# Performance work log

Measured on AMD Instinct MI355X. Metric: run time of the kernel, lower is better.

## Reference

```python
import jax, jax.numpy as jnp
import numpy as np

D_MODEL = 96
N_HEAD = 3
HEAD_DIM = D_MODEL // N_HEAD  # 32
D_FF = 2048
WIDTH = 65
HALF_W = (WIDTH - 1) // 2  # 32
EPS = 1e-5


def layer_norm(x, g, b):
    mu = jnp.mean(x, axis=-1, keepdims=True)
    var = jnp.mean(jnp.square(x - mu), axis=-1, keepdims=True)
    return (x - mu) * jax.lax.rsqrt(var + EPS) * g + b


def setup_inputs() -> dict:
    key = jax.random.key(0)
    ks = jax.random.split(key, 8)
    B, T = 8, 2048
    s = 0.05
    return {
        "x": jax.random.normal(ks[0], (B, D_MODEL, T), dtype=jnp.float32),
        "w_qkv": jax.random.normal(ks[1], (3 * D_MODEL, D_MODEL), dtype=jnp.float32) * s,
        "b_qkv": jnp.zeros((3 * D_MODEL,), dtype=jnp.float32),
        "w_out": jax.random.normal(ks[2], (D_MODEL, D_MODEL), dtype=jnp.float32) * s,
        "b_out": jnp.zeros((D_MODEL,), dtype=jnp.float32),
        "ln1_g": jnp.ones((D_MODEL,), dtype=jnp.float32),
        "ln1_b": jnp.zeros((D_MODEL,), dtype=jnp.float32),
        "w_ff1": jax.random.normal(ks[3], (D_FF, D_MODEL), dtype=jnp.float32) * s,
        "b_ff1": jnp.zeros((D_FF,), dtype=jnp.float32),
        "w_ff2": jax.random.normal(ks[4], (D_MODEL, D_FF), dtype=jnp.float32) * s,
        "b_ff2": jnp.zeros((D_MODEL,), dtype=jnp.float32),
        "ln2_g": jnp.ones((D_MODEL,), dtype=jnp.float32),
        "ln2_b": jnp.zeros((D_MODEL,), dtype=jnp.float32),
        "lnf_g": jnp.ones((D_MODEL,), dtype=jnp.float32),
        "lnf_b": jnp.zeros((D_MODEL,), dtype=jnp.float32),
    }


def reference(x, w_qkv, b_qkv, w_out, b_out, ln1_g, ln1_b, w_ff1, b_ff1,
              w_ff2, b_ff2, ln2_g, ln2_b, lnf_g, lnf_b):
    # x: (B, C, T) -> (B, T, C)
    h = jnp.transpose(x, (0, 2, 1))
    B, T, C = h.shape

    # --- multi-head self-attention with banded mask ---
    qkv = h @ w_qkv.T + b_qkv                      # (B, T, 3C)
    q, k, v = jnp.split(qkv, 3, axis=-1)
    q = q.reshape(B, T, N_HEAD, HEAD_DIM)
    k = k.reshape(B, T, N_HEAD, HEAD_DIM)
    v = v.reshape(B, T, N_HEAD, HEAD_DIM)

    scale = 1.0 / jnp.sqrt(jnp.float32(HEAD_DIM))
    scores = jnp.einsum("bthd,bshd->bhts", q, k) * scale  # (B, H, T, T)

    idx = jnp.arange(T)
    band = jnp.abs(idx[:, None] - idx[None, :]) <= HALF_W  # |i-j| <= half width
    scores = jnp.where(band[None, None], scores, jnp.float32(-jnp.inf))

    attn = jax.nn.softmax(scores, axis=-1)
    ctx = jnp.einsum("bhts,bshd->bthd", attn, v).reshape(B, T, C)
    attn_out = ctx @ w_out.T + b_out

    # --- post-norm encoder layer (dropout inactive / eval mode) ---
    h = layer_norm(h + attn_out, ln1_g, ln1_b)
    ff = jax.nn.relu(h @ w_ff1.T + b_ff1) @ w_ff2.T + b_ff2
    h = layer_norm(h + ff, ln2_g, ln2_b)

    # extra layernorm applied when width is not None
    h = layer_norm(h, lnf_g, lnf_b)

    # (B, T, C) -> (B, C, T)
    return jnp.transpose(h, (0, 2, 1))
```

## Files before the change

### kernel.cpp

```cpp
#include <hip/hip_runtime.h>
#include <hip/hip_bf16.h>

#define B 8
#define T 2048
#define C 96
#define NH 3
#define HD 32
#define FFD 2048
#define HALF_W 32
#define BT (B*T)
#define NT 384

typedef __hip_bfloat16 bf16;
typedef __attribute__((ext_vector_type(8))) short short8;
typedef __attribute__((ext_vector_type(4))) short short4v;
typedef __attribute__((ext_vector_type(16))) float floatx16;

__device__ __forceinline__ short f2bs(float v){
    __hip_bfloat16 h = __float2bfloat16(v);
    return *reinterpret_cast<short*>(&h);
}
__device__ __forceinline__ float bs2f(short s){
    unsigned u = ((unsigned)(unsigned short)s) << 16;
    return __uint_as_float(u);
}
__device__ __forceinline__ short8 ld_b64x2(const short* p){
    short4v a = *(const short4v*)p;
    short4v b = *(const short4v*)(p + 4);
    short8 v;
    v[0]=a[0]; v[1]=a[1]; v[2]=a[2]; v[3]=a[3];
    v[4]=b[0]; v[5]=b[1]; v[6]=b[2]; v[7]=b[3];
    return v;
}
__device__ __forceinline__ int4 exch_pair(int a0,int a1,int b0,int b1,int hq){
    int ra0=__shfl_xor(a0,32), ra1=__shfl_xor(a1,32);
    int rb0=__shfl_xor(b0,32), rb1=__shfl_xor(b1,32);
    int4 s;
    s.x = hq ? rb0 : a0;
    s.y = hq ? rb1 : a1;
    s.z = hq ? b0  : ra0;
    s.w = hq ? b1  : ra1;
    return s;
}
__device__ __forceinline__ void proj_pack(const floatx16& acc, const float* bias32, int hq,
                                          short8& f0, short8& f1){
    int pkq[4][2];
    #pragma unroll
    for(int q = 0; q < 4; ++q){
        float4 bv = *(const float4*)(bias32 + 8*q + 4*hq);
        short4v t;
        t[0]=f2bs(acc[4*q+0]+bv.x); t[1]=f2bs(acc[4*q+1]+bv.y);
        t[2]=f2bs(acc[4*q+2]+bv.z); t[3]=f2bs(acc[4*q+3]+bv.w);
        int2 u = *(int2*)&t; pkq[q][0]=u.x; pkq[q][1]=u.y;
    }
    int4 r0 = exch_pair(pkq[0][0],pkq[0][1],pkq[1][0],pkq[1][1],hq);
    int4 r1 = exch_pair(pkq[2][0],pkq[2][1],pkq[3][0],pkq[3][1],hq);
    f0 = *(short8*)&r0; f1 = *(short8*)&r1;
}

__global__ void cvtw_kernel(const float* __restrict__ wq, const float* __restrict__ wo,
                            const float* __restrict__ w1, const float* __restrict__ w2,
                            bf16* __restrict__ dst){
    int i = blockIdx.x*256 + threadIdx.x;
    if(i < 27648){
        int e = i&7, lane = (i>>3)&63, r = i>>9;
        int ks = r%6, ot = r/6;
        int o = ot*32 + (lane&31);
        int k = ks*16 + (lane>>5)*8 + e;
        dst[i] = __float2bfloat16(wq[o*96 + k]);
    } else if(i < 36864){
        int j = i - 27648;
        int e = j&7, lane = (j>>3)&63, r = j>>9;
        int ks = r%6, ct = r/6;
        int c = ct*32 + (lane&31);
        int k = ks*16 + (lane>>5)*8 + e;
        dst[i] = __float2bfloat16(wo[c*96 + k]);
    } else if(i < 233472){
        int j = i - 36864;
        int e = j&7, lane = (j>>3)&63, r = j>>9;
        int ks = r%6; r /= 6;
        int w = r%4, jt = r/4;
        int row = jt*128 + w*32 + (lane&31);
        int k = ks*16 + (lane>>5)*8 + e;
        dst[i] = __float2bfloat16(w1[row*96 + k]);
    } else if(i < 430080){
        int j = i - 233472;
        int e = j&7, lane = (j>>3)&63, r = j>>9;
        int ct = r%3; r /= 3;
        int g = r%2; r /= 2;
        int w = r%4, jt = r/4;
        int c = ct*32 + (lane&31);
        int k = jt*128 + w*32 + g*16 + (lane>>5)*8 + e;
        dst[i] = __float2bfloat16(w2[c*FFD + k]);
    }
}

__global__ __launch_bounds__(384, 3) void encoder_kernel(
    const float* __restrict__ x,
    const bf16* __restrict__ wqs, const bf16* __restrict__ wos,
    const bf16* __restrict__ w1s, const bf16* __restrict__ w2s,
    const float* __restrict__ b_qkv, const float* __restrict__ b_out,
    const float* __restrict__ g1, const float* __restrict__ bb1,
    const float* __restrict__ b1, const float* __restrict__ b2,
    const float* __restrict__ g2, const float* __restrict__ bt2,
    const float* __restrict__ gf, const float* __restrict__ btf,
    float* __restrict__ out){
    __shared__ __align__(16) char smem[59392];
    short* XS   = (short*)smem;
    short* PTS  = (short*)smem;
    float* REDP = (float*)smem;
    short* VTS  = (short*)(smem + 26112);
    float* ZT   = (float*)(smem + 26112);
    short* CTX  = (short*)(smem + 45312);
    short* H1S  = (short*)(smem + 51712);
    float* LSS  = (float*)(smem + 58112);
    float* RED1 = (float*)(smem + 58496);

    const int tid = threadIdx.x;
    const int u = tid >> 6, lane = tid & 63;
    const int lm = lane & 31, hq = lane >> 5;
    const int grp = u / 3, h = u % 3;
    const int b  = blockIdx.x >> 6;
    const int tt = blockIdx.x & 63;
    const int t0 = tt * 32;
    const float* xb = x + (size_t)b*C*T;

    int tg0 = t0 - 32;
    if(tg0 >= 0 && t0 + 64 <= T){
        for(int e = tid; e < 96*24; e += NT){
            int c = e / 24, t4 = e % 24;
            float4 v = *(const float4*)(xb + (size_t)c*T + tg0 + t4*4);
            XS[(t4*4+0)*104 + c] = f2bs(v.x);
            XS[(t4*4+1)*104 + c] = f2bs(v.y);
            XS[(t4*4+2)*104 + c] = f2bs(v.z);
            XS[(t4*4+3)*104 + c] = f2bs(v.w);
        }
    } else {
        for(int e = tid; e < 96*96; e += NT){
            int c = e / 96, j = e % 96;
            int t = tg0 + j; t = t < 0 ? 0 : (t > T-1 ? T-1 : t);
            XS[j*104 + c] = f2bs(xb[(size_t)c*T + t]);
        }
    }
    __syncthreads();

    short8 kf[3][2], qf0, qf1, wof[6];
    if(grp == 0){
        short8 kwf[6];
        #pragma unroll
        for(int ks = 0; ks < 6; ++ks)
            kwf[ks] = *(const short8*)((const short*)wqs + (size_t)((3+h)*6 + ks)*512 + lane*8);
        #pragma unroll
        for(int tau = 0; tau < 3; ++tau){
            short8 bfr[6];
            #pragma unroll
            for(int ks = 0; ks < 6; ++ks)
                bfr[ks] = *(const short8*)(XS + (tau*32+lm)*104 + ks*16 + hq*8);
            floatx16 acc;
            #pragma unroll
            for(int r = 0; r < 16; ++r) acc[r] = 0.f;
            #pragma unroll
            for(int ks = 0; ks < 6; ++ks)
                acc = __builtin_amdgcn_mfma_f32_32x32x16_bf16(kwf[ks], bfr[ks], acc, 0,0,0);
            proj_pack(acc, b_qkv + (3+h)*32, hq, kf[tau][0], kf[tau][1]);
            if(tau == 1){
                floatx16 qa;
                #pragma unroll
                for(int r = 0; r < 16; ++r) qa[r] = 0.f;
                #pragma unroll
                for(int ks = 0; ks < 6; ++ks){
                    short8 qwf = *(const short8*)((const short*)wqs + (size_t)(h*6 + ks)*512 + lane*8);
                    qa = __builtin_amdgcn_mfma_f32_32x32x16_bf16(qwf, bfr[ks], qa, 0,0,0);
                }
                proj_pack(qa, b_qkv + h*32, hq, qf0, qf1);
            }
        }
        #pragma unroll
        for(int ks = 0; ks < 6; ++ks)
            wof[ks] = *(const short8*)((const short*)wos + (size_t)(h*6 + ks)*512 + lane*8);
    } else {
        short8 vwf[6];
        #pragma unroll
        for(int ks = 0; ks < 6; ++ks)
            vwf[ks] = *(const short8*)((const short*)wqs + (size_t)((6+h)*6 + ks)*512 + lane*8);
        #pragma unroll
        for(int tau = 0; tau < 3; ++tau){
            short8 bfr[6];
            #pragma unroll
            for(int ks = 0; ks < 6; ++ks)
                bfr[ks] = *(const short8*)(XS + (tau*32+lm)*104 + ks*16 + hq*8);
            floatx16 acc;
            #pragma unroll
            for(int r = 0; r < 16; ++r) acc[r] = 0.f;
            #pragma unroll
            for(int ks = 0; ks < 6; ++ks)
                acc = __builtin_amdgcn_mfma_f32_32x32x16_bf16(vwf[ks], bfr[ks], acc, 0,0,0);
            #pragma unroll
            for(int q = 0; q < 4; ++q){
                float4 bv = *(const float4*)(b_qkv + (6+h)*32 + 8*q + 4*hq);
                float bva[4] = {bv.x, bv.y, bv.z, bv.w};
                #pragma unroll
                for(int r = 0; r < 4; ++r)
                    VTS[h*3200 + (8*q + 4*hq + r)*100 + tau*32 + lm] = f2bs(acc[4*q+r] + bva[r]);
            }
        }
    }
    __syncthreads();

    if(grp == 0){
        floatx16 S[3];
        #pragma unroll
        for(int sub = 0; sub < 3; ++sub){
            floatx16 z;
            #pragma unroll
            for(int r = 0; r < 16; ++r) z[r] = 0.f;
            z = __builtin_amdgcn_mfma_f32_32x32x16_bf16(kf[sub][0], qf0, z, 0,0,0);
            z = __builtin_amdgcn_mfma_f32_32x32x16_bf16(kf[sub][1], qf1, z, 0,0,0);
            S[sub] = z;
        }
        const float scale = 0.17677669529663687f;
        float part = 0.f;
        #pragma unroll
        for(int sub = 0; sub < 3; ++sub){
            #pragma unroll
            for(int r = 0; r < 16; ++r){
                int key_local = sub*32 + (r&3) + 8*(r>>2) + 4*hq;
                int s_glob = t0 - 32 + key_local;
                int rel = key_local - lm;
                bool ok = (rel >= 0) && (rel <= 64) && (s_glob >= 0) && (s_glob < T);
                float p = ok ? __expf(S[sub][r]*scale) : 0.f;
                S[sub][r] = p;
                part += p;
            }
        }
        float ltot = part + __shfl_xor(part, 32);
        if(hq == 0) LSS[h*32 + lm] = ltot;
        #pragma unroll
        for(int sub = 0; sub < 3; ++sub){
            #pragma unroll
            for(int q4 = 0; q4 < 4; ++q4){
                int kbase = sub*32 + 8*q4 + 4*hq;
                short4v pk4;
                pk4[0] = f2bs(S[sub][4*q4+0]);
                pk4[1] = f2bs(S[sub][4*q4+1]);
                pk4[2] = f2bs(S[sub][4*q4+2]);
                pk4[3] = f2bs(S[sub][4*q4+3]);
                *(short4v*)(PTS + h*3200 + lm*100 + kbase) = pk4;
            }
        }
        floatx16 O;
        #pragma unroll
        for(int r = 0; r < 16; ++r) O[r] = 0.f;
        #pragma unroll
        for(int ks = 0; ks < 6; ++ks){
            short8 pa = ld_b64x2(PTS + h*3200 + lm*100 + ks*16 + hq*8);
            short8 vf = ld_b64x2(VTS + h*3200 + lm*100 + ks*16 + hq*8);
            O = __builtin_amdgcn_mfma_f32_32x32x16_bf16(pa, vf, O, 0,0,0);
        }
        #pragma unroll
        for(int r = 0; r < 16; ++r){
            int qr = (r&3) + 8*(r>>2) + 4*hq;
            float linv = 1.f / LSS[h*32 + qr];
            CTX[qr*100 + h*32 + lm] = f2bs(O[r]*linv);
        }
    }
    __syncthreads();

    float vals[16];
    if(grp == 0){
        short8 cbfr[6];
        #pragma unroll
        for(int ks = 0; ks < 6; ++ks)
            cbfr[ks] = ld_b64x2(CTX + lm*100 + ks*16 + hq*8);
        floatx16 pacc;
        #pragma unroll
        for(int r = 0; r < 16; ++r) pacc[r] = 0.f;
        #pragma unroll
        for(int ks = 0; ks < 6; ++ks)
            pacc = __builtin_amdgcn_mfma_f32_32x32x16_bf16(wof[ks], cbfr[ks], pacc, 0,0,0);
        float p1 = 0.f, p2 = 0.f;
        #pragma unroll
        for(int q = 0; q < 4; ++q){
            int c = h*32 + 8*q + 4*hq;
            float4 bv = *(const float4*)(b_out + c);
            float bva[4] = {bv.x, bv.y, bv.z, bv.w};
            #pragma unroll
            for(int r = 0; r < 4; ++r){
                float xv = xb[(size_t)(c + r)*T + t0 + lm];
                float v = pacc[4*q+r] + bva[r] + xv;
                vals[4*q+r] = v;
                p1 += v; p2 += v*v;
            }
        }
        p1 += __shfl_xor(p1, 32);
        p2 += __shfl_xor(p2, 32);
        if(hq == 0){ RED1[h*32 + lm] = p1; RED1[96 + h*32 + lm] = p2; }
    }
    __syncthreads();
    if(grp == 0){
        float s  = RED1[lm] + RED1[32 + lm] + RED1[64 + lm];
        float s2 = RED1[96 + lm] + RED1[128 + lm] + RED1[160 + lm];
        float mu = s * (1.0f/96.0f);
        float rstd = rsqrtf(s2*(1.0f/96.0f) - mu*mu + 1e-5f);
        #pragma unroll
        for(int q = 0; q < 4; ++q){
            int c = h*32 + 8*q + 4*hq;
            float4 gv = *(const float4*)(g1 + c);
            float4 bv = *(const float4*)(bb1 + c);
            float ga[4] = {gv.x, gv.y, gv.z, gv.w};
            float ba[4] = {bv.x, bv.y, bv.z, bv.w};
            short4v pkv;
            #pragma unroll
            for(int r = 0; r < 4; ++r)
                pkv[r] = f2bs((vals[4*q+r] - mu)*rstd*ga[r] + ba[r]);
            *(short4v*)(H1S + lm*100 + c) = pkv;
        }
    }
    __syncthreads();

    short8 hf[6];
    #pragma unroll
    for(int ks = 0; ks < 6; ++ks)
        hf[ks] = ld_b64x2(H1S + lm*100 + ks*16 + hq*8);
    floatx16 acc2[3];
    #pragma unroll
    for(int i = 0; i < 3; ++i)
        #pragma unroll
        for(int r = 0; r < 16; ++r) acc2[i][r] = 0.f;
    const short* w1b = (const short*)w1s + lane*8;
    const short* w2b = (const short*)w2s + lane*8;
    short8 cw1[6];
    #pragma unroll
    for(int ks = 0; ks < 6; ++ks)
        cw1[ks] = *(const short8*)(w1b + (size_t)(u*6 + ks)*512);
    const int nJ = (u < 4) ? 11 : 10;
    for(int it = 0; it < nJ; ++it){
        const int J  = u + it*6;
        const int Jn = (J + 6 < 64) ? J + 6 : u;
        short8 nw1[6];
        #pragma unroll
        for(int ks = 0; ks < 6; ++ks)
            nw1[ks] = *(const short8*)(w1b + (size_t)(Jn*6 + ks)*512);
        short8 w2f[6];
        #pragma unroll
        for(int g = 0; g < 2; ++g)
            #pragma unroll
            for(int ct = 0; ct < 3; ++ct)
                w2f[g*3 + ct] = *(const short8*)(w2b + (size_t)((J*2 + g)*3 + ct)*512);
        floatx16 a0;
        #pragma unroll
        for(int r = 0; r < 16; ++r) a0[r] = 0.f;
        #pragma unroll
        for(int ks = 0; ks < 6; ++ks)
            a0 = __builtin_amdgcn_mfma_f32_32x32x16_bf16(cw1[ks], hf[ks], a0, 0,0,0);
        int pk[4][2];
        #pragma unroll
        for(int q = 0; q < 4; ++q){
            float4 bv = *(const float4*)(b1 + J*32 + 8*q + 4*hq);
            float bva[4] = {bv.x, bv.y, bv.z, bv.w};
            short4v tv;
            #pragma unroll
            for(int r = 0; r < 4; ++r){
                float v0 = a0[4*q+r] + bva[r];
                tv[r] = f2bs(v0 > 0.f ? v0 : 0.f);
            }
            int2 uu = *(int2*)&tv; pk[q][0] = uu.x; pk[q][1] = uu.y;
        }
        #pragma unroll
        for(int g = 0; g < 2; ++g){
            int4 sfi = exch_pair(pk[2*g][0], pk[2*g][1], pk[2*g+1][0], pk[2*g+1][1], hq);
            short8 sf = *(short8*)&sfi;
            #pragma unroll
            for(int ct = 0; ct < 3; ++ct)
                acc2[ct] = __builtin_amdgcn_mfma_f32_32x32x16_bf16(w2f[g*3+ct], sf, acc2[ct], 0,0,0);
        }
        #pragma unroll
        for(int ks = 0; ks < 6; ++ks) cw1[ks] = nw1[ks];
    }

    float fv[16];
    float e1 = 0.f, e2 = 0.f;
    for(int s = 0; s < 3; ++s){
        #pragma unroll
        for(int q = 0; q < 4; ++q)
            #pragma unroll
            for(int r = 0; r < 4; ++r)
                REDP[u*1088 + lane*17 + 4*q + r] = acc2[s][4*q+r];
        __syncthreads();
        if(u == s){
            #pragma unroll
            for(int q = 0; q < 4; ++q){
                int c = s*32 + 8*q + 4*hq;
                float4 bv = *(const float4*)(b2 + c);
                float bva[4] = {bv.x, bv.y, bv.z, bv.w};
                #pragma unroll
                for(int r = 0; r < 4; ++r){
                    float v = REDP[0*1088 + lane*17 + 4*q + r]
                            + REDP[1*1088 + lane*17 + 4*q + r]
                            + REDP[2*1088 + lane*17 + 4*q + r]
                            + REDP[3*1088 + lane*17 + 4*q + r]
                            + REDP[4*1088 + lane*17 + 4*q + r]
                            + REDP[5*1088 + lane*17 + 4*q + r]
                            + bva[r] + bs2f(H1S[lm*100 + c + r]);
                    fv[4*q+r] = v;
                    e1 += v; e2 += v*v;
                }
            }
        }
        __syncthreads();
    }
    if(grp == 0){
        e1 += __shfl_xor(e1, 32);
        e2 += __shfl_xor(e2, 32);
        if(hq == 0){ RED1[h*32 + lm] = e1; RED1[96 + h*32 + lm] = e2; }
    }
    __syncthreads();
    float f1 = 0.f, f2 = 0.f;
    if(grp == 0){
        float s  = RED1[lm] + RED1[32 + lm] + RED1[64 + lm];
        float s2 = RED1[96 + lm] + RED1[128 + lm] + RED1[160 + lm];
        float mu = s * (1.0f/96.0f);
        float rstd = rsqrtf(s2*(1.0f/96.0f) - mu*mu + 1e-5f);
        #pragma unroll
        for(int q = 0; q < 4; ++q){
            int c = h*32 + 8*q + 4*hq;
            float4 gv = *(const float4*)(g2 + c);
            float4 bv = *(const float4*)(bt2 + c);
            float ga[4] = {gv.x, gv.y, gv.z, gv.w};
            float ba[4] = {bv.x, bv.y, bv.z, bv.w};
            #pragma unroll
            for(int r = 0; r < 4; ++r){
                float y = (fv[4*q+r] - mu)*rstd*ga[r] + ba[r];
                fv[4*q+r] = y;
                f1 += y; f2 += y*y;
            }
        }
        f1 += __shfl_xor(f1, 32);
        f2 += __shfl_xor(f2, 32);
    }
    __syncthreads();
    if(grp == 0 && hq == 0){ RED1[h*32 + lm] = f1; RED1[96 + h*32 + lm] = f2; }
    __syncthreads();
    if(grp == 0){
        float s  = RED1[lm] + RED1[32 + lm] + RED1[64 + lm];
        float s2 = RED1[96 + lm] + RED1[128 + lm] + RED1[160 + lm];
        float mu = s * (1.0f/96.0f);
        float rstd = rsqrtf(s2*(1.0f/96.0f) - mu*mu + 1e-5f);
        #pragma unroll
        for(int q = 0; q < 4; ++q){
            int c = h*32 + 8*q + 4*hq;
            float4 gv = *(const float4*)(gf + c);
            float4 bv = *(const float4*)(btf + c);
            float ga[4] = {gv.x, gv.y, gv.z, gv.w};
            float ba[4] = {bv.x, bv.y, bv.z, bv.w};
            #pragma unroll
            for(int r = 0; r < 4; ++r)
                ZT[(c + r)*36 + lm] = (fv[4*q+r] - mu)*rstd*ga[r] + ba[r];
        }
    }
    __syncthreads();
    float* ob = out + (size_t)b*C*T + t0;
    for(int e = tid; e < 96*8; e += NT){
        int c = e >> 3, qq = e & 7;
        *(float4*)(ob + (size_t)c*T + qq*4) = *(const float4*)(ZT + c*36 + qq*4);
    }
}

extern "C" void kernel_launch(void* const* d_in, const int* in_sizes, int n_in,
                              void* d_out, int out_size, void* d_ws, size_t ws_size,
                              hipStream_t stream) {
    const float* x     = (const float*)d_in[0];
    const float* w_qkv = (const float*)d_in[1];
    const float* b_qkv = (const float*)d_in[2];
    const float* w_out = (const float*)d_in[3];
    const float* b_out = (const float*)d_in[4];
    const float* ln1_g = (const float*)d_in[5];
    const float* ln1_b = (const float*)d_in[6];
    const float* w_ff1 = (const float*)d_in[7];
    const float* b_ff1 = (const float*)d_in[8];
    const float* w_ff2 = (const float*)d_in[9];
    const float* b_ff2 = (const float*)d_in[10];
    const float* ln2_g = (const float*)d_in[11];
    const float* ln2_b = (const float*)d_in[12];
    const float* lnf_g = (const float*)d_in[13];
    const float* lnf_b = (const float*)d_in[14];
    float* out = (float*)d_out;

    bf16* wts = (bf16*)d_ws;
    bf16* wqs = wts;
    bf16* wos = wts + 27648;
    bf16* w1s = wts + 36864;
    bf16* w2s = wts + 233472;

    cvtw_kernel   <<<1680, 256, 0, stream>>>(w_qkv, w_out, w_ff1, w_ff2, wts);
    encoder_kernel<<<B*(T/32), NT, 0, stream>>>(x, wqs, wos, w1s, w2s,
                                                b_qkv, b_out, ln1_g, ln1_b,
                                                b_ff1, b_ff2, ln2_g, ln2_b,
                                                lnf_g, lnf_b, out);
}
```

Measured before the change: 135.7 us.

## Double block to 12 waves, split QKV work and reduce FFN partials via atomics

Raises the block from 6 to 12 waves, with four waves per head that share the K, Q and V projections, staging K in shared memory. The FFN hidden tiles are spread across 12 waves, so each wave handles about half as many. The cross-wave reduction of FFN outputs now uses shared-memory atomicAdd into a zeroed buffer instead of three staged reduction rounds with barriers, and the shared-memory footprint shrinks. The aim is more parallelism per tile and fewer barriers. In exchange it adds LDS atomic contention, extra syncs, and pressure from launch_bounds(768,6) on registers.

```diff
diff --git a/kernel.cpp b/kernel.cpp
--- a/kernel.cpp
+++ b/kernel.cpp
@@ -9,7 +9,7 @@
 #define FFD 2048
 #define HALF_W 32
 #define BT (B*T)
-#define NT 384
+#define NT 768
 
 typedef __hip_bfloat16 bf16;
 typedef __attribute__((ext_vector_type(8))) short short8;
@@ -95,7 +95,7 @@
     }
 }
 
-__global__ __launch_bounds__(384, 3) void encoder_kernel(
+__global__ __launch_bounds__(768, 6) void encoder_kernel(
     const float* __restrict__ x,
     const bf16* __restrict__ wqs, const bf16* __restrict__ wos,
     const bf16* __restrict__ w1s, const bf16* __restrict__ w2s,
@@ -105,21 +105,22 @@
     const float* __restrict__ g2, const float* __restrict__ bt2,
     const float* __restrict__ gf, const float* __restrict__ btf,
     float* __restrict__ out){
-    __shared__ __align__(16) char smem[59392];
+    __shared__ __align__(16) char smem[53120];
     short* XS   = (short*)smem;
     short* PTS  = (short*)smem;
-    float* REDP = (float*)smem;
-    short* VTS  = (short*)(smem + 26112);
-    float* ZT   = (float*)(smem + 26112);
-    short* CTX  = (short*)(smem + 45312);
-    short* H1S  = (short*)(smem + 51712);
-    float* LSS  = (float*)(smem + 58112);
-    float* RED1 = (float*)(smem + 58496);
+    short* KS   = (short*)(smem + 19968);
+    short* CTX  = (short*)(smem + 19968);
+    short* H1S  = (short*)(smem + 26368);
+    short* VTS  = (short*)(smem + 32768);
+    float* FVS  = (float*)(smem + 32768);
+    float* ZT   = (float*)(smem + 32768);
+    float* LSS  = (float*)(smem + 51968);
+    float* RED1 = (float*)(smem + 52352);
 
     const int tid = threadIdx.x;
     const int u = tid >> 6, lane = tid & 63;
     const int lm = lane & 31, hq = lane >> 5;
-    const int grp = u / 3, h = u % 3;
+    const int p = u & 3, h = u >> 2;
     const int b  = blockIdx.x >> 6;
     const int tt = blockIdx.x & 63;
     const int t0 = tt * 32;
@@ -144,14 +145,21 @@
     }
     __syncthreads();
 
-    short8 kf[3][2], qf0, qf1, wof[6];
-    if(grp == 0){
+    short8 wof[6];
+    if(u < 3){
+        #pragma unroll
+        for(int ks = 0; ks < 6; ++ks)
+            wof[ks] = *(const short8*)((const short*)wos + (size_t)(u*6 + ks)*512 + lane*8);
+    }
+
+    short8 kf2[2], qf0, qf1;
+    if(p == 0){
         short8 kwf[6];
         #pragma unroll
         for(int ks = 0; ks < 6; ++ks)
             kwf[ks] = *(const short8*)((const short*)wqs + (size_t)((3+h)*6 + ks)*512 + lane*8);
         #pragma unroll
-        for(int tau = 0; tau < 3; ++tau){
+        for(int tau = 0; tau < 2; ++tau){
             short8 bfr[6];
             #pragma unroll
             for(int ks = 0; ks < 6; ++ks)
@@ -162,29 +170,54 @@
             #pragma unroll
             for(int ks = 0; ks < 6; ++ks)
                 acc = __builtin_amdgcn_mfma_f32_32x32x16_bf16(kwf[ks], bfr[ks], acc, 0,0,0);
-            proj_pack(acc, b_qkv + (3+h)*32, hq, kf[tau][0], kf[tau][1]);
-            if(tau == 1){
-                floatx16 qa;
-                #pragma unroll
-                for(int r = 0; r < 16; ++r) qa[r] = 0.f;
-                #pragma unroll
-                for(int ks = 0; ks < 6; ++ks){
-                    short8 qwf = *(const short8*)((const short*)wqs + (size_t)(h*6 + ks)*512 + lane*8);
-                    qa = __builtin_amdgcn_mfma_f32_32x32x16_bf16(qwf, bfr[ks], qa, 0,0,0);
-                }
-                proj_pack(qa, b_qkv + h*32, hq, qf0, qf1);
-            }
-        }
-        #pragma unroll
-        for(int ks = 0; ks < 6; ++ks)
-            wof[ks] = *(const short8*)((const short*)wos + (size_t)(h*6 + ks)*512 + lane*8);
+            short8 f0, f1;
+            proj_pack(acc, b_qkv + (3+h)*32, hq, f0, f1);
+            short* kp = KS + (size_t)(h*2 + tau)*1024 + lane*8;
+            *(short8*)kp = f0;
+            *(short8*)(kp + 512) = f1;
+        }
+    } else if(p == 1){
+        short8 kwf[6];
+        #pragma unroll
+        for(int ks = 0; ks < 6; ++ks)
+            kwf[ks] = *(const short8*)((const short*)wqs + (size_t)((3+h)*6 + ks)*512 + lane*8);
+        {
+            short8 bfr[6];
+            #pragma unroll
+            for(int ks = 0; ks < 6; ++ks)
+                bfr[ks] = *(const short8*)(XS + (2*32+lm)*104 + ks*16 + hq*8);
+            floatx16 acc;
+            #pragma unroll
+            for(int r = 0; r < 16; ++r) acc[r] = 0.f;
+            #pragma unroll
+            for(int ks = 0; ks < 6; ++ks)
+                acc = __builtin_amdgcn_mfma_f32_32x32x16_bf16(kwf[ks], bfr[ks], acc, 0,0,0);
+            proj_pack(acc, b_qkv + (3+h)*32, hq, kf2[0], kf2[1]);
+        }
+        {
+            short8 bfr[6];
+            #pragma unroll
+            for(int ks = 0; ks < 6; ++ks)
+                bfr[ks] = *(const short8*)(XS + (1*32+lm)*104 + ks*16 + hq*8);
+            floatx16 qa;
+            #pragma unroll
+            for(int r = 0; r < 16; ++r) qa[r] = 0.f;
+            #pragma unroll
+            for(int ks = 0; ks < 6; ++ks){
+                short8 qwf = *(const short8*)((const short*)wqs + (size_t)(h*6 + ks)*512 + lane*8);
+                qa = __builtin_amdgcn_mfma_f32_32x32x16_bf16(qwf, bfr[ks], qa, 0,0,0);
+            }
+            proj_pack(qa, b_qkv + h*32, hq, qf0, qf1);
+        }
     } else {
         short8 vwf[6];
         #pragma unroll
         for(int ks = 0; ks < 6; ++ks)
             vwf[ks] = *(const short8*)((const short*)wqs + (size_t)((6+h)*6 + ks)*512 + lane*8);
-        #pragma unroll
-        for(int tau = 0; tau < 3; ++tau){
+        const int taua = (p == 2) ? 0 : 2;
+        const int ntau = (p == 2) ? 2 : 1;
+        for(int i = 0; i < ntau; ++i){
+            int tau = taua + i;
             short8 bfr[6];
             #pragma unroll
             for(int ks = 0; ks < 6; ++ks)
@@ -207,15 +240,22 @@
     }
     __syncthreads();
 
-    if(grp == 0){
+    float on[16];
+    if(p == 1){
         floatx16 S[3];
         #pragma unroll
         for(int sub = 0; sub < 3; ++sub){
+            short8 ka, kb;
+            if(sub < 2){
+                const short* kp = KS + (size_t)(h*2 + sub)*1024 + lane*8;
+                ka = *(const short8*)kp;
+                kb = *(const short8*)(kp + 512);
+            } else { ka = kf2[0]; kb = kf2[1]; }
             floatx16 z;
             #pragma unroll
             for(int r = 0; r < 16; ++r) z[r] = 0.f;
-            z = __builtin_amdgcn_mfma_f32_32x32x16_bf16(kf[sub][0], qf0, z, 0,0,0);
-            z = __builtin_amdgcn_mfma_f32_32x32x16_bf16(kf[sub][1], qf1, z, 0,0,0);
+            z = __builtin_amdgcn_mfma_f32_32x32x16_bf16(ka, qf0, z, 0,0,0);
+            z = __builtin_amdgcn_mfma_f32_32x32x16_bf16(kb, qf1, z, 0,0,0);
             S[sub] = z;
         }
         const float scale = 0.17677669529663687f;
@@ -228,9 +268,9 @@
                 int s_glob = t0 - 32 + key_local;
                 int rel = key_local - lm;
                 bool ok = (rel >= 0) && (rel <= 64) && (s_glob >= 0) && (s_glob < T);
-                float p = ok ? __expf(S[sub][r]*scale) : 0.f;
-                S[sub][r] = p;
-                part += p;
+                float pe = ok ? __expf(S[sub][r]*scale) : 0.f;
+                S[sub][r] = pe;
+                part += pe;
             }
         }
         float ltot = part + __shfl_xor(part, 32);
@@ -260,14 +300,24 @@
         #pragma unroll
         for(int r = 0; r < 16; ++r){
             int qr = (r&3) + 8*(r>>2) + 4*hq;
-            float linv = 1.f / LSS[h*32 + qr];
-            CTX[qr*100 + h*32 + lm] = f2bs(O[r]*linv);
-        }
-    }
-    __syncthreads();
-
+            on[r] = O[r] / LSS[h*32 + qr];
+        }
+    }
+    __syncthreads();
+    if(p == 1){
+        #pragma unroll
+        for(int r = 0; r < 16; ++r){
+            int qr = (r&3) + 8*(r>>2) + 4*hq;
+            CTX[qr*100 + h*32 + lm] = f2bs(on[r]);
+        }
+    }
+    __syncthreads();
+
+    if(u >= 3){
+        for(int i = tid - 192; i < 96*33; i += 576) FVS[i] = 0.f;
+    }
     float vals[16];
-    if(grp == 0){
+    if(u < 3){
         short8 cbfr[6];
         #pragma unroll
         for(int ks = 0; ks < 6; ++ks)
@@ -281,7 +331,7 @@
         float p1 = 0.f, p2 = 0.f;
         #pragma unroll
         for(int q = 0; q < 4; ++q){
-            int c = h*32 + 8*q + 4*hq;
+            int c = u*32 + 8*q + 4*hq;
             float4 bv = *(const float4*)(b_out + c);
             float bva[4] = {bv.x, bv.y, bv.z, bv.w};
             #pragma unroll
@@ -294,17 +344,17 @@
         }
         p1 += __shfl_xor(p1, 32);
         p2 += __shfl_xor(p2, 32);
-        if(hq == 0){ RED1[h*32 + lm] = p1; RED1[96 + h*32 + lm] = p2; }
-    }
-    __syncthreads();
-    if(grp == 0){
+        if(hq == 0){ RED1[u*32 + lm] = p1; RED1[96 + u*32 + lm] = p2; }
+    }
+    __syncthreads();
+    if(u < 3){
         float s  = RED1[lm] + RED1[32 + lm] + RED1[64 + lm];
         float s2 = RED1[96 + lm] + RED1[128 + lm] + RED1[160 + lm];
         float mu = s * (1.0f/96.0f);
         float rstd = rsqrtf(s2*(1.0f/96.0f) - mu*mu + 1e-5f);
         #pragma unroll
         for(int q = 0; q < 4; ++q){
-            int c = h*32 + 8*q + 4*hq;
+            int c = u*32 + 8*q + 4*hq;
             float4 gv = *(const float4*)(g1 + c);
             float4 bv = *(const float4*)(bb1 + c);
             float ga[4] = {gv.x, gv.y, gv.z, gv.w};
@@ -333,10 +383,10 @@
     #pragma unroll
     for(int ks = 0; ks < 6; ++ks)
         cw1[ks] = *(const short8*)(w1b + (size_t)(u*6 + ks)*512);
-    const int nJ = (u < 4) ? 11 : 10;
+    const int nJ = (u < 4) ? 6 : 5;
     for(int it = 0; it < nJ; ++it){
-        const int J  = u + it*6;
-        const int Jn = (J + 6 < 64) ? J + 6 : u;
+        const int J  = u + it*12;
+        const int Jn = (J + 12 < 64) ? J + 12 : u;
         short8 nw1[6];
         #pragma unroll
         for(int ks = 0; ks < 6; ++ks)
@@ -377,53 +427,46 @@
         #pragma unroll
         for(int ks = 0; ks < 6; ++ks) cw1[ks] = nw1[ks];
     }
+    #pragma unroll
+    for(int ct = 0; ct < 3; ++ct)
+        #pragma unroll
+        for(int q = 0; q < 4; ++q)
+            #pragma unroll
+            for(int r = 0; r < 4; ++r){
+                int c = ct*32 + 8*q + 4*hq + r;
+                atomicAdd(&FVS[c*33 + lm], acc2[ct][4*q+r]);
+            }
+    __syncthreads();
 
     float fv[16];
     float e1 = 0.f, e2 = 0.f;
-    for(int s = 0; s < 3; ++s){
-        #pragma unroll
-        for(int q = 0; q < 4; ++q)
-            #pragma unroll
-            for(int r = 0; r < 4; ++r)
-                REDP[u*1088 + lane*17 + 4*q + r] = acc2[s][4*q+r];
-        __syncthreads();
-        if(u == s){
-            #pragma unroll
-            for(int q = 0; q < 4; ++q){
-                int c = s*32 + 8*q + 4*hq;
-                float4 bv = *(const float4*)(b2 + c);
-                float bva[4] = {bv.x, bv.y, bv.z, bv.w};
-                #pragma unroll
-                for(int r = 0; r < 4; ++r){
-                    float v = REDP[0*1088 + lane*17 + 4*q + r]
-                            + REDP[1*1088 + lane*17 + 4*q + r]
-                            + REDP[2*1088 + lane*17 + 4*q + r]
-                            + REDP[3*1088 + lane*17 + 4*q + r]
-                            + REDP[4*1088 + lane*17 + 4*q + r]
-                            + REDP[5*1088 + lane*17 + 4*q + r]
-                            + bva[r] + bs2f(H1S[lm*100 + c + r]);
-                    fv[4*q+r] = v;
-                    e1 += v; e2 += v*v;
-                }
-            }
-        }
-        __syncthreads();
-    }
-    if(grp == 0){
+    if(u < 3){
+        #pragma unroll
+        for(int q = 0; q < 4; ++q){
+            int cb = u*32 + 8*q + 4*hq;
+            float4 bv = *(const float4*)(b2 + cb);
+            float bva[4] = {bv.x, bv.y, bv.z, bv.w};
+            #pragma unroll
+            for(int r = 0; r < 4; ++r){
+                float v = FVS[(cb + r)*33 + lm] + bva[r] + bs2f(H1S[lm*100 + cb + r]);
+                fv[4*q+r] = v;
+                e1 += v; e2 += v*v;
+            }
+        }
         e1 += __shfl_xor(e1, 32);
         e2 += __shfl_xor(e2, 32);
-        if(hq == 0){ RED1[h*32 + lm] = e1; RED1[96 + h*32 + lm] = e2; }
+        if(hq == 0){ RED1[u*32 + lm] = e1; RED1[96 + u*32 + lm] = e2; }
     }
     __syncthreads();
     float f1 = 0.f, f2 = 0.f;
-    if(grp == 0){
+    if(u < 3){
         float s  = RED1[lm] + RED1[32 + lm] + RED1[64 + lm];
         float s2 = RED1[96 + lm] + RED1[128 + lm] + RED1[160 + lm];
         float mu = s * (1.0f/96.0f);
         float rstd = rsqrtf(s2*(1.0f/96.0f) - mu*mu + 1e-5f);
         #pragma unroll
         for(int q = 0; q < 4; ++q){
-            int c = h*32 + 8*q + 4*hq;
+            int c = u*32 + 8*q + 4*hq;
             float4 gv = *(const float4*)(g2 + c);
             float4 bv = *(const float4*)(bt2 + c);
             float ga[4] = {gv.x, gv.y, gv.z, gv.w};
@@ -439,16 +482,16 @@
         f2 += __shfl_xor(f2, 32);
     }
     __syncthreads();
-    if(grp == 0 && hq == 0){ RED1[h*32 + lm] = f1; RED1[96 + h*32 + lm] = f2; }
-    __syncthreads();
-    if(grp == 0){
+    if(u < 3 && hq == 0){ RED1[u*32 + lm] = f1; RED1[96 + u*32 + lm] = f2; }
+    __syncthreads();
+    if(u < 3){
         float s  = RED1[lm] + RED1[32 + lm] + RED1[64 + lm];
         float s2 = RED1[96 + lm] + RED1[128 + lm] + RED1[160 + lm];
         float mu = s * (1.0f/96.0f);
         float rstd = rsqrtf(s2*(1.0f/96.0f) - mu*mu + 1e-5f);
         #pragma unroll
         for(int q = 0; q < 4; ++q){
-            int c = h*32 + 8*q + 4*hq;
+            int c = u*32 + 8*q + 4*hq;
             float4 gv = *(const float4*)(gf + c);
             float4 bv = *(const float4*)(btf + c);
             float ga[4] = {gv.x, gv.y, gv.z, gv.w};
```

New measurement: 279.8 us. 106% more time.

## Split fused encoder into attention and feed-forward kernels via bf16 intermediate

Applied to the files above, without the earlier changes.

The single fused kernel is split in two. An attention kernel (occupancy hint raised to 4) writes the LayerNorm-1 output as bf16 rows to workspace. A feed-forward kernel with 512 threads then processes 64 rows per block, reusing each loaded W1/W2 fragment across two 32-row tiles, with eight waves splitting the FFD range. Partial sums are combined through LDS atomics instead of the staged REDP reduction. The aim is to halve weight traffic per row and raise occupancy, at the cost of an extra global round-trip, a second launch, and fewer blocks (256) for the FF stage.

```diff
diff --git a/kernel.cpp b/kernel.cpp
--- a/kernel.cpp
+++ b/kernel.cpp
@@ -9,7 +9,6 @@
 #define FFD 2048
 #define HALF_W 32
 #define BT (B*T)
-#define NT 384
 
 typedef __hip_bfloat16 bf16;
 typedef __attribute__((ext_vector_type(8))) short short8;
@@ -95,56 +94,56 @@
     }
 }
 
-__global__ __launch_bounds__(384, 3) void encoder_kernel(
+__global__ __launch_bounds__(384, 4) void attn_kernel(
     const float* __restrict__ x,
     const bf16* __restrict__ wqs, const bf16* __restrict__ wos,
-    const bf16* __restrict__ w1s, const bf16* __restrict__ w2s,
     const float* __restrict__ b_qkv, const float* __restrict__ b_out,
     const float* __restrict__ g1, const float* __restrict__ bb1,
-    const float* __restrict__ b1, const float* __restrict__ b2,
-    const float* __restrict__ g2, const float* __restrict__ bt2,
-    const float* __restrict__ gf, const float* __restrict__ btf,
-    float* __restrict__ out){
-    __shared__ __align__(16) char smem[59392];
+    bf16* __restrict__ h1b){
+    __shared__ __align__(16) char smem[45952];
     short* XS   = (short*)smem;
     short* PTS  = (short*)smem;
-    float* REDP = (float*)smem;
-    short* VTS  = (short*)(smem + 26112);
-    float* ZT   = (float*)(smem + 26112);
-    short* CTX  = (short*)(smem + 45312);
-    short* H1S  = (short*)(smem + 51712);
-    float* LSS  = (float*)(smem + 58112);
-    float* RED1 = (float*)(smem + 58496);
+    short* VTS  = (short*)(smem + 19200);
+    short* CTX  = (short*)(smem + 38400);
+    float* LSS  = (float*)(smem + 44800);
+    float* RED1 = (float*)(smem + 45184);
 
     const int tid = threadIdx.x;
     const int u = tid >> 6, lane = tid & 63;
     const int lm = lane & 31, hq = lane >> 5;
     const int grp = u / 3, h = u % 3;
-    const int b  = blockIdx.x >> 6;
-    const int tt = blockIdx.x & 63;
+    const int b  = blockIdx.x & 7;
+    const int tt = blockIdx.x >> 3;
     const int t0 = tt * 32;
     const float* xb = x + (size_t)b*C*T;
 
     int tg0 = t0 - 32;
     if(tg0 >= 0 && t0 + 64 <= T){
-        for(int e = tid; e < 96*24; e += NT){
+        for(int e = tid; e < 96*24; e += 384){
             int c = e / 24, t4 = e % 24;
             float4 v = *(const float4*)(xb + (size_t)c*T + tg0 + t4*4);
-            XS[(t4*4+0)*104 + c] = f2bs(v.x);
-            XS[(t4*4+1)*104 + c] = f2bs(v.y);
-            XS[(t4*4+2)*104 + c] = f2bs(v.z);
-            XS[(t4*4+3)*104 + c] = f2bs(v.w);
+            XS[(t4*4+0)*100 + c] = f2bs(v.x);
+            XS[(t4*4+1)*100 + c] = f2bs(v.y);
+            XS[(t4*4+2)*100 + c] = f2bs(v.z);
+            XS[(t4*4+3)*100 + c] = f2bs(v.w);
         }
     } else {
-        for(int e = tid; e < 96*96; e += NT){
+        for(int e = tid; e < 96*96; e += 384){
             int c = e / 96, j = e % 96;
             int t = tg0 + j; t = t < 0 ? 0 : (t > T-1 ? T-1 : t);
-            XS[j*104 + c] = f2bs(xb[(size_t)c*T + t]);
-        }
-    }
-    __syncthreads();
-
-    short8 kf[3][2], qf0, qf1, wof[6];
+            XS[j*100 + c] = f2bs(xb[(size_t)c*T + t]);
+        }
+    }
+    __syncthreads();
+
+    short8 wof[6];
+    if(u < 3){
+        #pragma unroll
+        for(int ks = 0; ks < 6; ++ks)
+            wof[ks] = *(const short8*)((const short*)wos + (size_t)(u*6 + ks)*512 + lane*8);
+    }
+
+    short8 kf[3][2], qf0, qf1;
     if(grp == 0){
         short8 kwf[6];
         #pragma unroll
@@ -155,7 +154,7 @@
             short8 bfr[6];
             #pragma unroll
             for(int ks = 0; ks < 6; ++ks)
-                bfr[ks] = *(const short8*)(XS + (tau*32+lm)*104 + ks*16 + hq*8);
+                bfr[ks] = *(const short8*)(XS + (tau*32+lm)*100 + ks*16 + hq*8);
             floatx16 acc;
             #pragma unroll
             for(int r = 0; r < 16; ++r) acc[r] = 0.f;
@@ -175,9 +174,6 @@
                 proj_pack(qa, b_qkv + h*32, hq, qf0, qf1);
             }
         }
-        #pragma unroll
-        for(int ks = 0; ks < 6; ++ks)
-            wof[ks] = *(const short8*)((const short*)wos + (size_t)(h*6 + ks)*512 + lane*8);
     } else {
         short8 vwf[6];
         #pragma unroll
@@ -188,7 +184,7 @@
             short8 bfr[6];
             #pragma unroll
             for(int ks = 0; ks < 6; ++ks)
-                bfr[ks] = *(const short8*)(XS + (tau*32+lm)*104 + ks*16 + hq*8);
+                bfr[ks] = *(const short8*)(XS + (tau*32+lm)*100 + ks*16 + hq*8);
             floatx16 acc;
             #pragma unroll
             for(int r = 0; r < 16; ++r) acc[r] = 0.f;
@@ -228,9 +224,9 @@
                 int s_glob = t0 - 32 + key_local;
                 int rel = key_local - lm;
                 bool ok = (rel >= 0) && (rel <= 64) && (s_glob >= 0) && (s_glob < T);
-                float p = ok ? __expf(S[sub][r]*scale) : 0.f;
-                S[sub][r] = p;
-                part += p;
+                float pe = ok ? __expf(S[sub][r]*scale) : 0.f;
+                S[sub][r] = pe;
+                part += pe;
             }
         }
         float ltot = part + __shfl_xor(part, 32);
@@ -267,7 +263,7 @@
     __syncthreads();
 
     float vals[16];
-    if(grp == 0){
+    if(u < 3){
         short8 cbfr[6];
         #pragma unroll
         for(int ks = 0; ks < 6; ++ks)
@@ -281,7 +277,7 @@
         float p1 = 0.f, p2 = 0.f;
         #pragma unroll
         for(int q = 0; q < 4; ++q){
-            int c = h*32 + 8*q + 4*hq;
+            int c = u*32 + 8*q + 4*hq;
             float4 bv = *(const float4*)(b_out + c);
             float bva[4] = {bv.x, bv.y, bv.z, bv.w};
             #pragma unroll
@@ -294,17 +290,18 @@
         }
         p1 += __shfl_xor(p1, 32);
         p2 += __shfl_xor(p2, 32);
-        if(hq == 0){ RED1[h*32 + lm] = p1; RED1[96 + h*32 + lm] = p2; }
-    }
-    __syncthreads();
-    if(grp == 0){
+        if(hq == 0){ RED1[u*32 + lm] = p1; RED1[96 + u*32 + lm] = p2; }
+    }
+    __syncthreads();
+    if(u < 3){
         float s  = RED1[lm] + RED1[32 + lm] + RED1[64 + lm];
         float s2 = RED1[96 + lm] + RED1[128 + lm] + RED1[160 + lm];
         float mu = s * (1.0f/96.0f);
         float rstd = rsqrtf(s2*(1.0f/96.0f) - mu*mu + 1e-5f);
+        int row = b*T + t0 + lm;
         #pragma unroll
         for(int q = 0; q < 4; ++q){
-            int c = h*32 + 8*q + 4*hq;
+            int c = u*32 + 8*q + 4*hq;
             float4 gv = *(const float4*)(g1 + c);
             float4 bv = *(const float4*)(bb1 + c);
             float ga[4] = {gv.x, gv.y, gv.z, gv.w};
@@ -313,117 +310,145 @@
             #pragma unroll
             for(int r = 0; r < 4; ++r)
                 pkv[r] = f2bs((vals[4*q+r] - mu)*rstd*ga[r] + ba[r]);
-            *(short4v*)(H1S + lm*100 + c) = pkv;
-        }
-    }
-    __syncthreads();
-
-    short8 hf[6];
+            *(short4v*)((short*)h1b + (size_t)row*96 + c) = pkv;
+        }
+    }
+}
+
+__global__ __launch_bounds__(512, 2) void ff_kernel(
+    const bf16* __restrict__ h1b,
+    const bf16* __restrict__ w1s, const float* __restrict__ b1,
+    const bf16* __restrict__ w2s, const float* __restrict__ b2,
+    const float* __restrict__ g2, const float* __restrict__ bt2,
+    const float* __restrict__ gf, const float* __restrict__ btf,
+    float* __restrict__ out){
+    __shared__ __align__(16) char smem[29184];
+    float* FVS  = (float*)smem;
+    float* RED1 = (float*)(smem + 26112);
+    float* RED2 = (float*)(smem + 27648);
+
+    const int tid = threadIdx.x;
+    const int u = tid >> 6, lane = tid & 63;
+    const int lm = lane & 31, hq = lane >> 5;
+    const int r0 = blockIdx.x * 64;
+    const short* h1p = (const short*)h1b;
+
+    short8 hf[2][6];
     #pragma unroll
-    for(int ks = 0; ks < 6; ++ks)
-        hf[ks] = ld_b64x2(H1S + lm*100 + ks*16 + hq*8);
-    floatx16 acc2[3];
+    for(int mt = 0; mt < 2; ++mt)
+        #pragma unroll
+        for(int ks = 0; ks < 6; ++ks)
+            hf[mt][ks] = *(const short8*)(h1p + (size_t)(r0 + mt*32 + lm)*96 + ks*16 + hq*8);
+
+    for(int i = tid; i < 96*68; i += 512) FVS[i] = 0.f;
+
+    floatx16 acc2[2][3];
     #pragma unroll
-    for(int i = 0; i < 3; ++i)
-        #pragma unroll
-        for(int r = 0; r < 16; ++r) acc2[i][r] = 0.f;
+    for(int mt = 0; mt < 2; ++mt)
+        #pragma unroll
+        for(int i = 0; i < 3; ++i)
+            #pragma unroll
+            for(int r = 0; r < 16; ++r) acc2[mt][i][r] = 0.f;
+
     const short* w1b = (const short*)w1s + lane*8;
     const short* w2b = (const short*)w2s + lane*8;
-    short8 cw1[6];
-    #pragma unroll
-    for(int ks = 0; ks < 6; ++ks)
-        cw1[ks] = *(const short8*)(w1b + (size_t)(u*6 + ks)*512);
-    const int nJ = (u < 4) ? 11 : 10;
-    for(int it = 0; it < nJ; ++it){
-        const int J  = u + it*6;
-        const int Jn = (J + 6 < 64) ? J + 6 : u;
-        short8 nw1[6];
-        #pragma unroll
-        for(int ks = 0; ks < 6; ++ks)
-            nw1[ks] = *(const short8*)(w1b + (size_t)(Jn*6 + ks)*512);
-        short8 w2f[6];
+    __syncthreads();
+
+    #pragma unroll 2
+    for(int it = 0; it < 8; ++it){
+        const int J = u + it*8;
+        short8 cw1[6], w2f[6];
+        #pragma unroll
+        for(int ks = 0; ks < 6; ++ks)
+            cw1[ks] = *(const short8*)(w1b + (size_t)(J*6 + ks)*512);
         #pragma unroll
         for(int g = 0; g < 2; ++g)
             #pragma unroll
             for(int ct = 0; ct < 3; ++ct)
                 w2f[g*3 + ct] = *(const short8*)(w2b + (size_t)((J*2 + g)*3 + ct)*512);
-        floatx16 a0;
-        #pragma unroll
-        for(int r = 0; r < 16; ++r) a0[r] = 0.f;
-        #pragma unroll
-        for(int ks = 0; ks < 6; ++ks)
-            a0 = __builtin_amdgcn_mfma_f32_32x32x16_bf16(cw1[ks], hf[ks], a0, 0,0,0);
-        int pk[4][2];
+        floatx16 a0, a1;
+        #pragma unroll
+        for(int r = 0; r < 16; ++r){ a0[r] = 0.f; a1[r] = 0.f; }
+        #pragma unroll
+        for(int ks = 0; ks < 6; ++ks){
+            a0 = __builtin_amdgcn_mfma_f32_32x32x16_bf16(cw1[ks], hf[0][ks], a0, 0,0,0);
+            a1 = __builtin_amdgcn_mfma_f32_32x32x16_bf16(cw1[ks], hf[1][ks], a1, 0,0,0);
+        }
+        int pk[2][4][2];
         #pragma unroll
         for(int q = 0; q < 4; ++q){
             float4 bv = *(const float4*)(b1 + J*32 + 8*q + 4*hq);
             float bva[4] = {bv.x, bv.y, bv.z, bv.w};
-            short4v tv;
+            short4v t0v, t1v;
             #pragma unroll
             for(int r = 0; r < 4; ++r){
                 float v0 = a0[4*q+r] + bva[r];
-                tv[r] = f2bs(v0 > 0.f ? v0 : 0.f);
-            }
-            int2 uu = *(int2*)&tv; pk[q][0] = uu.x; pk[q][1] = uu.y;
+                float v1 = a1[4*q+r] + bva[r];
+                t0v[r] = f2bs(v0 > 0.f ? v0 : 0.f);
+                t1v[r] = f2bs(v1 > 0.f ? v1 : 0.f);
+            }
+            int2 u0 = *(int2*)&t0v; int2 u1 = *(int2*)&t1v;
+            pk[0][q][0] = u0.x; pk[0][q][1] = u0.y;
+            pk[1][q][0] = u1.x; pk[1][q][1] = u1.y;
         }
         #pragma unroll
         for(int g = 0; g < 2; ++g){
-            int4 sfi = exch_pair(pk[2*g][0], pk[2*g][1], pk[2*g+1][0], pk[2*g+1][1], hq);
-            short8 sf = *(short8*)&sfi;
-            #pragma unroll
-            for(int ct = 0; ct < 3; ++ct)
-                acc2[ct] = __builtin_amdgcn_mfma_f32_32x32x16_bf16(w2f[g*3+ct], sf, acc2[ct], 0,0,0);
-        }
-        #pragma unroll
-        for(int ks = 0; ks < 6; ++ks) cw1[ks] = nw1[ks];
-    }
-
+            #pragma unroll
+            for(int mt = 0; mt < 2; ++mt){
+                int4 sfi = exch_pair(pk[mt][2*g][0], pk[mt][2*g][1],
+                                     pk[mt][2*g+1][0], pk[mt][2*g+1][1], hq);
+                short8 sf = *(short8*)&sfi;
+                #pragma unroll
+                for(int ct = 0; ct < 3; ++ct)
+                    acc2[mt][ct] = __builtin_amdgcn_mfma_f32_32x32x16_bf16(
+                                       w2f[g*3+ct], sf, acc2[mt][ct], 0,0,0);
+            }
+        }
+    }
+    #pragma unroll
+    for(int mt = 0; mt < 2; ++mt)
+        #pragma unroll
+        for(int ct = 0; ct < 3; ++ct)
+            #pragma unroll
+            for(int q = 0; q < 4; ++q)
+                #pragma unroll
+                for(int r = 0; r < 4; ++r){
+                    int c = ct*32 + 8*q + 4*hq + r;
+                    atomicAdd(&FVS[c*68 + mt*32 + lm], acc2[mt][ct][4*q+r]);
+                }
+    __syncthreads();
+
+    const int mt = u / 3, ct3 = u % 3;
     float fv[16];
     float e1 = 0.f, e2 = 0.f;
-    for(int s = 0; s < 3; ++s){
-        #pragma unroll
-        for(int q = 0; q < 4; ++q)
-            #pragma unroll
-            for(int r = 0; r < 4; ++r)
-                REDP[u*1088 + lane*17 + 4*q + r] = acc2[s][4*q+r];
-        __syncthreads();
-        if(u == s){
-            #pragma unroll
-            for(int q = 0; q < 4; ++q){
-                int c = s*32 + 8*q + 4*hq;
-                float4 bv = *(const float4*)(b2 + c);
-                float bva[4] = {bv.x, bv.y, bv.z, bv.w};
-                #pragma unroll
-                for(int r = 0; r < 4; ++r){
-                    float v = REDP[0*1088 + lane*17 + 4*q + r]
-                            + REDP[1*1088 + lane*17 + 4*q + r]
-                            + REDP[2*1088 + lane*17 + 4*q + r]
-                            + REDP[3*1088 + lane*17 + 4*q + r]
-                            + REDP[4*1088 + lane*17 + 4*q + r]
-                            + REDP[5*1088 + lane*17 + 4*q + r]
-                            + bva[r] + bs2f(H1S[lm*100 + c + r]);
-                    fv[4*q+r] = v;
-                    e1 += v; e2 += v*v;
-                }
-            }
-        }
-        __syncthreads();
-    }
-    if(grp == 0){
+    if(u < 6){
+        #pragma unroll
+        for(int q = 0; q < 4; ++q){
+            int cb = ct3*32 + 8*q + 4*hq;
+            float4 bv = *(const float4*)(b2 + cb);
+            float bva[4] = {bv.x, bv.y, bv.z, bv.w};
+            short4v hv = *(const short4v*)(h1p + (size_t)(r0 + mt*32 + lm)*96 + cb);
+            #pragma unroll
+            for(int r = 0; r < 4; ++r){
+                float v = FVS[(cb + r)*68 + mt*32 + lm] + bva[r] + bs2f(hv[r]);
+                fv[4*q+r] = v;
+                e1 += v; e2 += v*v;
+            }
+        }
         e1 += __shfl_xor(e1, 32);
         e2 += __shfl_xor(e2, 32);
-        if(hq == 0){ RED1[h*32 + lm] = e1; RED1[96 + h*32 + lm] = e2; }
-    }
-    __syncthreads();
-    float f1 = 0.f, f2 = 0.f;
-    if(grp == 0){
-        float s  = RED1[lm] + RED1[32 + lm] + RED1[64 + lm];
-        float s2 = RED1[96 + lm] + RED1[128 + lm] + RED1[160 + lm];
+        if(hq == 0){ RED1[mt*192 + ct3*32 + lm] = e1; RED1[mt*192 + 96 + ct3*32 + lm] = e2; }
+    }
+    __syncthreads();
+    if(u < 6){
+        float s  = RED1[mt*192 + lm] + RED1[mt*192 + 32 + lm] + RED1[mt*192 + 64 + lm];
+        float s2 = RED1[mt*192 + 96 + lm] + RED1[mt*192 + 128 + lm] + RED1[mt*192 + 160 + lm];
         float mu = s * (1.0f/96.0f);
         float rstd = rsqrtf(s2*(1.0f/96.0f) - mu*mu + 1e-5f);
+        float f1 = 0.f, f2 = 0.f;
         #pragma unroll
         for(int q = 0; q < 4; ++q){
-            int c = h*32 + 8*q + 4*hq;
+            int c = ct3*32 + 8*q + 4*hq;
             float4 gv = *(const float4*)(g2 + c);
             float4 bv = *(const float4*)(bt2 + c);
             float ga[4] = {gv.x, gv.y, gv.z, gv.w};
@@ -437,32 +462,32 @@
         }
         f1 += __shfl_xor(f1, 32);
         f2 += __shfl_xor(f2, 32);
-    }
-    __syncthreads();
-    if(grp == 0 && hq == 0){ RED1[h*32 + lm] = f1; RED1[96 + h*32 + lm] = f2; }
-    __syncthreads();
-    if(grp == 0){
-        float s  = RED1[lm] + RED1[32 + lm] + RED1[64 + lm];
-        float s2 = RED1[96 + lm] + RED1[128 + lm] + RED1[160 + lm];
+        if(hq == 0){ RED2[mt*192 + ct3*32 + lm] = f1; RED2[mt*192 + 96 + ct3*32 + lm] = f2; }
+    }
+    __syncthreads();
+    if(u < 6){
+        float s  = RED2[mt*192 + lm] + RED2[mt*192 + 32 + lm] + RED2[mt*192 + 64 + lm];
+        float s2 = RED2[mt*192 + 96 + lm] + RED2[mt*192 + 128 + lm] + RED2[mt*192 + 160 + lm];
         float mu = s * (1.0f/96.0f);
         float rstd = rsqrtf(s2*(1.0f/96.0f) - mu*mu + 1e-5f);
         #pragma unroll
         for(int q = 0; q < 4; ++q){
-            int c = h*32 + 8*q + 4*hq;
+            int c = ct3*32 + 8*q + 4*hq;
             float4 gv = *(const float4*)(gf + c);
             float4 bv = *(const float4*)(btf + c);
             float ga[4] = {gv.x, gv.y, gv.z, gv.w};
             float ba[4] = {bv.x, bv.y, bv.z, bv.w};
             #pragma unroll
             for(int r = 0; r < 4; ++r)
-                ZT[(c + r)*36 + lm] = (fv[4*q+r] - mu)*rstd*ga[r] + ba[r];
-        }
-    }
-    __syncthreads();
-    float* ob = out + (size_t)b*C*T + t0;
-    for(int e = tid; e < 96*8; e += NT){
-        int c = e >> 3, qq = e & 7;
-        *(float4*)(ob + (size_t)c*T + qq*4) = *(const float4*)(ZT + c*36 + qq*4);
+                FVS[(c + r)*68 + mt*32 + lm] = (fv[4*q+r] - mu)*rstd*ga[r] + ba[r];
+        }
+    }
+    __syncthreads();
+    const int bb = r0 / T, t0g = r0 % T;
+    float* ob = out + (size_t)bb*C*T + t0g;
+    for(int e = tid; e < 96*16; e += 512){
+        int c = e >> 4, tg = e & 15;
+        *(float4*)(ob + (size_t)c*T + tg*4) = *(const float4*)(FVS + c*68 + tg*4);
     }
 }
 
@@ -486,15 +511,17 @@
     const float* lnf_b = (const float*)d_in[14];
     float* out = (float*)d_out;
 
-    bf16* wts = (bf16*)d_ws;
+    char* wsb = (char*)d_ws;
+    bf16* wts = (bf16*)wsb;
     bf16* wqs = wts;
     bf16* wos = wts + 27648;
     bf16* w1s = wts + 36864;
     bf16* w2s = wts + 233472;
-
-    cvtw_kernel   <<<1680, 256, 0, stream>>>(w_qkv, w_out, w_ff1, w_ff2, wts);
-    encoder_kernel<<<B*(T/32), NT, 0, stream>>>(x, wqs, wos, w1s, w2s,
-                                                b_qkv, b_out, ln1_g, ln1_b,
-                                                b_ff1, b_ff2, ln2_g, ln2_b,
-                                                lnf_g, lnf_b, out);
-}
+    bf16* h1b = (bf16*)(wsb + 860160);
+
+    cvtw_kernel<<<1680, 256, 0, stream>>>(w_qkv, w_out, w_ff1, w_ff2, wts);
+    attn_kernel<<<512, 384, 0, stream>>>(x, wqs, wos, b_qkv, b_out,
+                                         ln1_g, ln1_b, h1b);
+    ff_kernel  <<<256, 512, 0, stream>>>(h1b, w1s, b_ff1, w2s, b_ff2,
+                                         ln2_g, ln2_b, lnf_g, lnf_b, out);
+}
```

Result: slower. 192.8 us (+42.1%).
